# Kernel optimization log

Hardware: AMD Instinct MI355X
Metric: run time of the kernel (lower is better)

## Reference

```python
import jax, jax.numpy as jnp
import numpy as np

N = 30000   # total nodes
E = 240000  # edges
B = 64      # graphs / proteins
H = 10      # GATv2 heads
C = 78      # per-head out dim (= xd_features)
D = H * C   # 780
SEQ = 1000
EMB = 128
LH = 64     # LSTM hidden per direction


def _lstm_dir(xs, Wih, Whh, bih, bhh, reverse):
    # xs: [T, Bn, EMB]; PyTorch gate order i,f,g,o
    Bn = xs.shape[1]
    h0 = jnp.zeros((Bn, LH), xs.dtype)
    def step(carry, xt):
        h, c = carry
        z = xt @ Wih.T + h @ Whh.T + bih + bhh
        i, f, g, o = jnp.split(z, 4, axis=-1)
        c = jax.nn.sigmoid(f) * c + jax.nn.sigmoid(i) * jnp.tanh(g)
        h = jax.nn.sigmoid(o) * jnp.tanh(c)
        return (h, c), h
    _, hs = jax.lax.scan(step, (h0, h0), xs, reverse=reverse)
    return hs


def setup_inputs() -> dict:
    k = jax.random.key(0)
    nxt = lambda i: jax.random.fold_in(k, i)
    s = 0.05
    d = {}
    d['x'] = jax.random.normal(nxt(0), (N, C), jnp.float32)
    d['edge_index'] = jax.random.randint(nxt(1), (2, E), 0, N)
    d['batch'] = jnp.sort(jax.random.randint(nxt(2), (N,), 0, B))
    d['target'] = jax.random.randint(nxt(3), (B, SEQ), 0, 26)
    # GATv2Conv params (share_weights=False)
    d['Wl'] = jax.random.normal(nxt(4), (C, D), jnp.float32) * s
    d['Wr'] = jax.random.normal(nxt(5), (C, D), jnp.float32) * s
    d['att'] = jax.random.normal(nxt(6), (H, C), jnp.float32) * s
    d['gat_b'] = jnp.zeros((D,), jnp.float32)
    # GCNConv params
    d['gcn_w'] = jax.random.normal(nxt(7), (D, D), jnp.float32) * s
    d['gcn_b'] = jnp.zeros((D,), jnp.float32)
    # protein branch
    d['emb'] = jax.random.normal(nxt(8), (26, EMB), jnp.float32) * s
    for tag, base in (('f', 9), ('b', 13)):
        d['Wih_' + tag] = jax.random.normal(nxt(base), (4 * LH, EMB), jnp.float32) * s
        d['Whh_' + tag] = jax.random.normal(nxt(base + 1), (4 * LH, LH), jnp.float32) * s
        d['bih_' + tag] = jnp.zeros((4 * LH,), jnp.float32)
        d['bhh_' + tag] = jnp.zeros((4 * LH,), jnp.float32)
    d['conv_w'] = jax.random.normal(nxt(17), (32, SEQ, 8), jnp.float32) * s
    d['conv_b'] = jnp.zeros((32,), jnp.float32)
    d['fcp_w'] = jax.random.normal(nxt(18), (32 * 121, 128), jnp.float32) * s
    d['fcp_b'] = jnp.zeros((128,), jnp.float32)
    # combined MLP (actual concat dim = 2*780 + 128 = 1688)
    d['fc1_w'] = jax.random.normal(nxt(19), (1688, 1024), jnp.float32) * s
    d['fc1_b'] = jnp.zeros((1024,), jnp.float32)
    d['fc2_w'] = jax.random.normal(nxt(20), (1024, 512), jnp.float32) * s
    d['fc2_b'] = jnp.zeros((512,), jnp.float32)
    d['out_w'] = jax.random.normal(nxt(21), (512, 1), jnp.float32) * s
    d['out_b'] = jnp.zeros((1,), jnp.float32)
    return d


def reference(x, edge_index, batch, target, Wl, Wr, att, gat_b, gcn_w, gcn_b,
              emb, Wih_f, Whh_f, bih_f, bhh_f, Wih_b, Whh_b, bih_b, bhh_b,
              conv_w, conv_b, fcp_w, fcp_b, fc1_w, fc1_b, fc2_w, fc2_b,
              out_w, out_b):
    # ---- graph branch (eval mode: dropout off) ----
    loops = jnp.arange(N)
    src = jnp.concatenate([edge_index[0], loops])  # self loops (PyG default)
    dst = jnp.concatenate([edge_index[1], loops])

    # GATv2Conv
    xl = (x @ Wl).reshape(N, H, C)
    xr = (x @ Wr).reshape(N, H, C)
    e = jax.nn.leaky_relu(xl[src] + xr[dst], 0.2)       # [E+N, H, C]
    logit = jnp.einsum('ehc,hc->eh', e, att)            # [E+N, H]
    m = jax.ops.segment_max(logit, dst, num_segments=N)
    ex = jnp.exp(logit - m[dst])
    den = jax.ops.segment_sum(ex, dst, num_segments=N)
    alpha = ex / den[dst]
    h = jax.ops.segment_sum(alpha[:, :, None] * xl[src], dst, num_segments=N)
    h = jax.nn.elu(h.reshape(N, D) + gat_b)

    # GCNConv with symmetric normalization
    hw = h @ gcn_w
    deg = jax.ops.segment_sum(jnp.ones_like(src, jnp.float32), dst, num_segments=N)
    dinv = jnp.where(deg > 0, jax.lax.rsqrt(jnp.maximum(deg, 1e-12)), 0.0)
    norm = dinv[src] * dinv[dst]
    g = jax.ops.segment_sum(norm[:, None] * hw[src], dst, num_segments=N) + gcn_b
    g = jax.nn.relu(g)

    # global max + mean pooling per graph
    gmax = jax.ops.segment_max(g, batch, num_segments=B)
    cnt = jax.ops.segment_sum(jnp.ones((N,), jnp.float32), batch, num_segments=B)
    gmean = jax.ops.segment_sum(g, batch, num_segments=B) / jnp.maximum(cnt, 1.0)[:, None]
    graph_feat = jnp.concatenate([gmax, gmean], axis=1)  # [B, 1560]

    # ---- protein branch ----
    et = emb[target]                                     # [B, SEQ, EMB]
    # nn.LSTM default batch_first=False: time axis is axis 0 (=B), batch axis is SEQ
    hf = _lstm_dir(et, Wih_f, Whh_f, bih_f, bhh_f, reverse=False)
    hb = _lstm_dir(et, Wih_b, Whh_b, bih_b, bhh_b, reverse=True)
    hcat = jnp.concatenate([hf, hb], axis=-1)            # [B, SEQ, 128]
    conv = jax.lax.conv_general_dilated(hcat, conv_w, (1,), 'VALID',
                                        dimension_numbers=('NCH', 'OIH', 'NCH'))
    conv = conv + conv_b[None, :, None]                  # [B, 32, 121]
    prot = conv.reshape(B, 32 * 121) @ fcp_w + fcp_b     # [B, 128]

    # ---- combined head ----
    comb = jnp.concatenate([graph_feat, prot], axis=1)   # [B, 1688]
    h1 = jax.nn.relu(comb @ fc1_w + fc1_b)
    h2 = jax.nn.relu(h1 @ fc2_w + fc2_b)
    return h2 @ out_w + out_b                            # [B, 1]
```

## Files before the change

### kernel.cpp

```cpp
#include <hip/hip_runtime.h>
#include <hip/hip_bf16.h>
#include <math.h>

static constexpr int NN   = 30000;
static constexpr int EE   = 240000;
static constexpr int ET   = EE + NN;
static constexpr int BB   = 64;
static constexpr int HH   = 10;
static constexpr int CC   = 78;
static constexpr int DD   = HH * CC;
static constexpr int SEQ  = 1000;
static constexpr int EMB  = 128;
static constexpr int LH   = 64;
static constexpr int COMBD = 2 * DD + 128;
static constexpr int PCHUNK = 64;

typedef __attribute__((ext_vector_type(8))) short short8;
typedef __attribute__((ext_vector_type(4))) float f32x4;

__device__ __forceinline__ float bf2f(unsigned short u) {
    return __uint_as_float(((unsigned int)u) << 16);
}

template <int OBF>
__global__ __launch_bounds__(256) void gemm_bf16_mfma(const __hip_bfloat16* __restrict__ A,
                                                      const __hip_bfloat16* __restrict__ Bt,
                                                      void* __restrict__ Cv,
                                                      int M, int N, int K) {
    constexpr int LDS_S = 40;
    __shared__ unsigned short As[128 * LDS_S];
    __shared__ unsigned short Bs[128 * LDS_S];
    const int tid  = threadIdx.x;
    const int lane = tid & 63, wid = tid >> 6;
    const int wr = wid >> 1, wc = wid & 1;
    const int l15 = lane & 15, l4 = lane >> 4;
    const int bm = blockIdx.y * 128, bn = blockIdx.x * 128;
    const int tr = tid >> 2, tc = (tid & 3) * 8;

    const unsigned short* Au = (const unsigned short*)A;
    const unsigned short* Bu = (const unsigned short*)Bt;

    f32x4 acc[4][4];
#pragma unroll
    for (int m = 0; m < 4; ++m)
#pragma unroll
        for (int n = 0; n < 4; ++n) acc[m][n] = (f32x4){0.f, 0.f, 0.f, 0.f};

    for (int k0 = 0; k0 < K; k0 += 32) {
#pragma unroll
        for (int half = 0; half < 2; ++half) {
            int row = tr + half * 64;
            {
                int grow = bm + row;
                short8 sv;
                if (grow < M && k0 + tc + 8 <= K) {
                    const unsigned int* p = (const unsigned int*)(Au + (size_t)grow * K + k0 + tc);
#pragma unroll
                    for (int j = 0; j < 4; ++j) {
                        unsigned int u = p[j];
                        sv[2 * j]     = (short)(u & 0xffffu);
                        sv[2 * j + 1] = (short)(u >> 16);
                    }
                } else {
#pragma unroll
                    for (int j = 0; j < 8; ++j) {
                        int gk = k0 + tc + j;
                        sv[j] = (grow < M && gk < K) ? (short)Au[(size_t)grow * K + gk] : (short)0;
                    }
                }
                *reinterpret_cast<short8*>(&As[row * LDS_S + tc]) = sv;
            }
            {
                int grow = bn + row;
                short8 sv;
                if (grow < N && k0 + tc + 8 <= K) {
                    const unsigned int* p = (const unsigned int*)(Bu + (size_t)grow * K + k0 + tc);
#pragma unroll
                    for (int j = 0; j < 4; ++j) {
                        unsigned int u = p[j];
                        sv[2 * j]     = (short)(u & 0xffffu);
                        sv[2 * j + 1] = (short)(u >> 16);
                    }
                } else {
#pragma unroll
                    for (int j = 0; j < 8; ++j) {
                        int gk = k0 + tc + j;
                        sv[j] = (grow < N && gk < K) ? (short)Bu[(size_t)grow * K + gk] : (short)0;
                    }
                }
                *reinterpret_cast<short8*>(&Bs[row * LDS_S + tc]) = sv;
            }
        }
        __syncthreads();
        short8 a[4], b[4];
#pragma unroll
        for (int m = 0; m < 4; ++m)
            a[m] = *reinterpret_cast<const short8*>(&As[(wr * 64 + m * 16 + l15) * LDS_S + l4 * 8]);
#pragma unroll
        for (int n = 0; n < 4; ++n)
            b[n] = *reinterpret_cast<const short8*>(&Bs[(wc * 64 + n * 16 + l15) * LDS_S + l4 * 8]);
#pragma unroll
        for (int m = 0; m < 4; ++m)
#pragma unroll
            for (int n = 0; n < 4; ++n)
                acc[m][n] = __builtin_amdgcn_mfma_f32_16x16x32_bf16(a[m], b[n], acc[m][n], 0, 0, 0);
        __syncthreads();
    }
#pragma unroll
    for (int m = 0; m < 4; ++m)
#pragma unroll
        for (int n = 0; n < 4; ++n)
#pragma unroll
            for (int r = 0; r < 4; ++r) {
                int row = bm + wr * 64 + m * 16 + l4 * 4 + r;
                int col = bn + wc * 64 + n * 16 + l15;
                if (row < M && col < N) {
                    if (OBF)
                        ((__hip_bfloat16*)Cv)[(size_t)row * N + col] = __float2bfloat16(acc[m][n][r]);
                    else
                        ((float*)Cv)[(size_t)row * N + col] = acc[m][n][r];
                }
            }
}

__global__ void f32_to_bf16(const float* __restrict__ in, __hip_bfloat16* __restrict__ out, int n) {
    int i = blockIdx.x * blockDim.x + threadIdx.x;
    if (i < n) out[i] = __float2bfloat16(in[i]);
}

__global__ void transpose_to_bf16(const float* __restrict__ in, __hip_bfloat16* __restrict__ out,
                                  int Kdim, int Ndim) {
    int idx = blockIdx.x * blockDim.x + threadIdx.x;
    if (idx >= Kdim * Ndim) return;
    int n = idx / Kdim, k = idx % Kdim;
    out[idx] = __float2bfloat16(in[(size_t)k * Ndim + n]);
}

__global__ void transpose_f32(const float* __restrict__ in, float* __restrict__ out,
                              int Kdim, int Ndim) {
    int idx = blockIdx.x * blockDim.x + threadIdx.x;
    if (idx >= Kdim * Ndim) return;
    int n = idx / Kdim, k = idx % Kdim;
    out[idx] = in[(size_t)k * Ndim + n];
}

template <int ACT>
__global__ __launch_bounds__(256) void gemm_skinny(const float* __restrict__ A,
                                                   const float* __restrict__ Bt,
                                                   const float* __restrict__ bias,
                                                   float* __restrict__ C,
                                                   int M, int N, int K, int ldc) {
    int oidx = blockIdx.x * 4 + (threadIdx.x >> 6);
    int lane = threadIdx.x & 63;
    if (oidx >= M * N) return;
    int row = oidx / N, col = oidx % N;
    const float4* a = (const float4*)(A + (size_t)row * K);
    const float4* b = (const float4*)(Bt + (size_t)col * K);
    int K4 = K >> 2;
    float s = 0.f;
    for (int i = lane; i < K4; i += 64) {
        float4 x = a[i], y = b[i];
        s += x.x * y.x + x.y * y.y + x.z * y.z + x.w * y.w;
    }
#pragma unroll
    for (int off = 32; off; off >>= 1) s += __shfl_xor(s, off);
    if (lane == 0) {
        s += bias[col];
        if (ACT == 1) s = fmaxf(s, 0.f);
        C[(size_t)row * ldc + col] = s;
    }
}

__global__ void deg_count(const int* __restrict__ ei, int* __restrict__ deg) {
    int e = blockIdx.x * blockDim.x + threadIdx.x;
    if (e >= ET) return;
    int d = (e < EE) ? ei[EE + e] : (e - EE);
    atomicAdd(&deg[d], 1);
}

__global__ __launch_bounds__(1024) void scan_kernel(const int* __restrict__ deg,
                                                    int* __restrict__ offs) {
    __shared__ int lds[1024];
    int tid = threadIdx.x;
    const int chunk = (NN + 1023) / 1024;
    int base = tid * chunk;
    int s = 0;
    for (int i = 0; i < chunk; ++i) {
        int idx = base + i;
        if (idx < NN) s += deg[idx];
    }
    lds[tid] = s;
    __syncthreads();
    for (int d = 1; d < 1024; d <<= 1) {
        int v = (tid >= d) ? lds[tid - d] : 0;
        __syncthreads();
        lds[tid] += v;
        __syncthreads();
    }
    int run = (tid == 0) ? 0 : lds[tid - 1];
    for (int i = 0; i < chunk; ++i) {
        int idx = base + i;
        if (idx < NN) { offs[idx] = run; run += deg[idx]; }
    }
    if (tid == 1023) offs[NN] = lds[1023];
}

__global__ void csr_fill(const int* __restrict__ ei, const int* __restrict__ offs,
                         int* __restrict__ cursor, int* __restrict__ csr_src,
                         int* __restrict__ csr_dst) {
    int e = blockIdx.x * blockDim.x + threadIdx.x;
    if (e >= ET) return;
    int s = (e < EE) ? ei[e] : (e - EE);
    int d = (e < EE) ? ei[EE + e] : (e - EE);
    int pos = atomicAdd(&cursor[d], 1);
    int slot = offs[d] + pos;
    csr_src[slot] = s;
    csr_dst[slot] = d;
}

__global__ void dinv_kernel(const int* __restrict__ deg, float* __restrict__ dinv) {
    int n = blockIdx.x * blockDim.x + threadIdx.x;
    if (n >= NN) return;
    float dg = (float)deg[n];
    dinv[n] = (dg > 0.f) ? 1.f / sqrtf(dg) : 0.f;
}

__global__ void gat_logits(const unsigned short* __restrict__ xl,
                           const unsigned short* __restrict__ xr,
                           const float* __restrict__ att, const int* __restrict__ csr_src,
                           const int* __restrict__ csr_dst, float* __restrict__ logit) {
    int idx = blockIdx.x * blockDim.x + threadIdx.x;
    if (idx >= ET * HH) return;
    int i = idx / HH, h = idx % HH;
    int s = csr_src[i], d = csr_dst[i];
    const unsigned int* pl = (const unsigned int*)(xl + (size_t)s * DD + h * CC);
    const unsigned int* pr = (const unsigned int*)(xr + (size_t)d * DD + h * CC);
    const float* pa = att + h * CC;
    float acc = 0.f;
#pragma unroll
    for (int c = 0; c < CC / 2; ++c) {
        unsigned int a = pl[c], b = pr[c];
        float v0 = __uint_as_float((a & 0xffffu) << 16) + __uint_as_float((b & 0xffffu) << 16);
        float v1 = __uint_as_float(a & 0xffff0000u) + __uint_as_float(b & 0xffff0000u);
        v0 = (v0 > 0.f) ? v0 : 0.2f * v0;
        v1 = (v1 > 0.f) ? v1 : 0.2f * v1;
        acc += pa[2 * c] * v0 + pa[2 * c + 1] * v1;
    }
    logit[idx] = acc;
}

__global__ void gat_softmax(const int* __restrict__ offs, float* __restrict__ logit) {
    int idx = blockIdx.x * blockDim.x + threadIdx.x;
    if (idx >= NN * HH) return;
    int n = idx / HH, h = idx % HH;
    int i0 = offs[n], i1 = offs[n + 1];
    float m = -1e30f;
    for (int i = i0; i < i1; ++i) m = fmaxf(m, logit[i * HH + h]);
    float den = 0.f;
    for (int i = i0; i < i1; ++i) {
        float e = expf(logit[i * HH + h] - m);
        logit[i * HH + h] = e;
        den += e;
    }
    float inv = 1.f / den;
    for (int i = i0; i < i1; ++i) logit[i * HH + h] *= inv;
}

__global__ __launch_bounds__(256) void gat_aggregate(const int* __restrict__ offs,
                                                     const int* __restrict__ csr_src,
                                                     const float* __restrict__ alpha,
                                                     const unsigned short* __restrict__ xl,
                                                     const float* __restrict__ gat_b,
                                                     __hip_bfloat16* __restrict__ hout) {
    int n = blockIdx.x;
    int tid = threadIdx.x;
    int i0 = offs[n], i1 = offs[n + 1];
    int d0 = tid, d1 = tid + 256, d2 = tid + 512, d3 = tid + 768;
    int h0 = d0 / CC, h1 = d1 / CC, h2 = d2 / CC, h3 = (d3 < DD) ? d3 / CC : 0;
    float a0 = 0.f, a1 = 0.f, a2 = 0.f, a3 = 0.f;
    for (int i = i0; i < i1; ++i) {
        const unsigned short* row = xl + (size_t)csr_src[i] * DD;
        const float* al = alpha + (size_t)i * HH;
        a0 += al[h0] * bf2f(row[d0]);
        a1 += al[h1] * bf2f(row[d1]);
        a2 += al[h2] * bf2f(row[d2]);
        if (d3 < DD) a3 += al[h3] * bf2f(row[d3]);
    }
    float v;
    v = a0 + gat_b[d0]; v = (v > 0.f) ? v : expf(v) - 1.f;
    hout[(size_t)n * DD + d0] = __float2bfloat16(v);
    v = a1 + gat_b[d1]; v = (v > 0.f) ? v : expf(v) - 1.f;
    hout[(size_t)n * DD + d1] = __float2bfloat16(v);
    v = a2 + gat_b[d2]; v = (v > 0.f) ? v : expf(v) - 1.f;
    hout[(size_t)n * DD + d2] = __float2bfloat16(v);
    if (d3 < DD) {
        v = a3 + gat_b[d3]; v = (v > 0.f) ? v : expf(v) - 1.f;
        hout[(size_t)n * DD + d3] = __float2bfloat16(v);
    }
}

__global__ __launch_bounds__(256) void gcn_aggregate(const int* __restrict__ offs,
                                                     const int* __restrict__ csr_src,
                                                     const float* __restrict__ dinv,
                                                     const unsigned short* __restrict__ hw,
                                                     const float* __restrict__ gcn_b,
                                                     __hip_bfloat16* __restrict__ g) {
    int n = blockIdx.x;
    int tid = threadIdx.x;
    float din = dinv[n];
    int i0 = offs[n], i1 = offs[n + 1];
    int d0 = tid, d1 = tid + 256, d2 = tid + 512, d3 = tid + 768;
    float a0 = 0.f, a1 = 0.f, a2 = 0.f, a3 = 0.f;
    for (int i = i0; i < i1; ++i) {
        int s = csr_src[i];
        float w = dinv[s] * din;
        const unsigned short* row = hw + (size_t)s * DD;
        a0 += w * bf2f(row[d0]);
        a1 += w * bf2f(row[d1]);
        a2 += w * bf2f(row[d2]);
        if (d3 < DD) a3 += w * bf2f(row[d3]);
    }
    g[(size_t)n * DD + d0] = __float2bfloat16(fmaxf(a0 + gcn_b[d0], 0.f));
    g[(size_t)n * DD + d1] = __float2bfloat16(fmaxf(a1 + gcn_b[d1], 0.f));
    g[(size_t)n * DD + d2] = __float2bfloat16(fmaxf(a2 + gcn_b[d2], 0.f));
    if (d3 < DD) g[(size_t)n * DD + d3] = __float2bfloat16(fmaxf(a3 + gcn_b[d3], 0.f));
}

__global__ void graph_ranges(const int* __restrict__ batch, int* __restrict__ gstart,
                             int* __restrict__ gend) {
    int n = blockIdx.x * blockDim.x + threadIdx.x;
    if (n >= NN) return;
    int b = batch[n];
    if (n == 0 || batch[n - 1] != b) gstart[b] = n;
    if (n == NN - 1 || batch[n + 1] != b) gend[b] = n + 1;
}

__global__ __launch_bounds__(256) void pool_partial(const unsigned short* __restrict__ g,
                                                    const int* __restrict__ batch,
                                                    float* __restrict__ pmax,
                                                    float* __restrict__ psum) {
    int chunk0 = blockIdx.x * PCHUNK;
    int tid = threadIdx.x;
    __shared__ int bsh[PCHUNK];
    for (int i = tid; i < PCHUNK; i += 256) {
        int n = chunk0 + i;
        bsh[i] = (n < NN) ? batch[n] : -1;
    }
    __syncthreads();
    float mx[4] = {0.f, 0.f, 0.f, 0.f};
    float sm[4] = {0.f, 0.f, 0.f, 0.f};
    int curb = bsh[0];
    auto flush = [&](int b) {
#pragma unroll
        for (int j = 0; j < 4; ++j) {
            int d = tid + j * 256;
            if (d < DD && b >= 0) {
                atomicMax((unsigned int*)&pmax[(size_t)b * DD + d], __float_as_uint(mx[j]));
                atomicAdd(&psum[(size_t)b * DD + d], sm[j]);
            }
            mx[j] = 0.f; sm[j] = 0.f;
        }
    };
    for (int i = 0; i < PCHUNK; ++i) {
        int n = chunk0 + i;
        if (n >= NN) break;
        int b = bsh[i];
        if (b != curb) { flush(curb); curb = b; }
        const unsigned short* row = g + (size_t)n * DD;
#pragma unroll
        for (int j = 0; j < 4; ++j) {
            int d = tid + j * 256;
            if (d < DD) {
                float v = bf2f(row[d]);
                mx[j] = fmaxf(mx[j], v);
                sm[j] += v;
            }
        }
    }
    flush(curb);
}

__global__ void pool_finalize(const float* __restrict__ pmax, const float* __restrict__ psum,
                              const int* __restrict__ gstart, const int* __restrict__ gend,
                              float* __restrict__ comb) {
    int idx = blockIdx.x * blockDim.x + threadIdx.x;
    if (idx >= BB * DD) return;
    int b = idx / DD, d = idx % DD;
    float cnt = fmaxf((float)(gend[b] - gstart[b]), 1.f);
    comb[(size_t)b * COMBD + d] = pmax[idx];
    comb[(size_t)b * COMBD + DD + d] = psum[idx] / cnt;
}

__global__ void proj26_kernel(const float* __restrict__ emb,
                              const float* __restrict__ Wih_f, const float* __restrict__ bih_f,
                              const float* __restrict__ bhh_f,
                              const float* __restrict__ Wih_b, const float* __restrict__ bih_b,
                              const float* __restrict__ bhh_b, float* __restrict__ proj) {
    int dir = blockIdx.x, row = blockIdx.y, j = threadIdx.x;
    const float* W = dir ? Wih_b : Wih_f;
    const float* b1 = dir ? bih_b : bih_f;
    const float* b2 = dir ? bhh_b : bhh_f;
    float acc = b1[j] + b2[j];
    const float* e = emb + row * EMB;
    const float* w = W + j * EMB;
    for (int k = 0; k < EMB; ++k) acc += e[k] * w[k];
    proj[(dir * 26 + row) * 256 + j] = acc;
}

__global__ __launch_bounds__(256) void lstm_kernel(const int* __restrict__ target,
                                                   const float* __restrict__ proj26,
                                                   const float* __restrict__ Whh_f,
                                                   const float* __restrict__ Whh_b,
                                                   float* __restrict__ hcat) {
    int n = blockIdx.x;
    int dir = blockIdx.y;
    int tid = threadIdx.x;
    const float* Whh = dir ? Whh_b : Whh_f;
    const float* proj = proj26 + dir * 26 * 256;
    float w[LH];
#pragma unroll
    for (int u4 = 0; u4 < LH / 4; ++u4) {
        float4 v = *reinterpret_cast<const float4*>(Whh + tid * LH + u4 * 4);
        w[u4 * 4 + 0] = v.x; w[u4 * 4 + 1] = v.y;
        w[u4 * 4 + 2] = v.z; w[u4 * 4 + 3] = v.w;
    }
    __shared__ float h_lds[LH];
    __shared__ float c_lds[LH];
    __shared__ float z_lds[256];
    if (tid < LH) { h_lds[tid] = 0.f; c_lds[tid] = 0.f; }
    __syncthreads();
    for (int s = 0; s < BB; ++s) {
        int t = dir ? (BB - 1 - s) : s;
        int tgt = target[t * SEQ + n];
        float a0 = 0.f, a1 = 0.f, a2 = 0.f, a3 = 0.f;
#pragma unroll
        for (int u = 0; u < LH; u += 4) {
            a0 += w[u] * h_lds[u];
            a1 += w[u + 1] * h_lds[u + 1];
            a2 += w[u + 2] * h_lds[u + 2];
            a3 += w[u + 3] * h_lds[u + 3];
        }
        z_lds[tid] = proj[tgt * 256 + tid] + a0 + a1 + a2 + a3;
        __syncthreads();
        if (tid < LH) {
            float ig = 1.f / (1.f + expf(-z_lds[tid]));
            float fg = 1.f / (1.f + expf(-z_lds[LH + tid]));
            float gg = tanhf(z_lds[2 * LH + tid]);
            float og = 1.f / (1.f + expf(-z_lds[3 * LH + tid]));
            float c = fg * c_lds[tid] + ig * gg;
            float h = og * tanhf(c);
            c_lds[tid] = c;
            h_lds[tid] = h;
            hcat[((size_t)t * SEQ + n) * 128 + dir * LH + tid] = h;
        }
        __syncthreads();
    }
}

__global__ __launch_bounds__(256) void transpose_hcat(const float* __restrict__ hcat,
                                                      unsigned short* __restrict__ hcatT) {
    int b = blockIdx.z;
    int i0 = blockIdx.y * 32;
    int h0 = blockIdx.x * 32;
    int th = threadIdx.x & 31;
    int ti = threadIdx.x >> 5;
    __shared__ float t[32][33];
#pragma unroll
    for (int r = 0; r < 4; ++r) {
        int i = i0 + ti + r * 8;
        if (i < SEQ) t[ti + r * 8][th] = hcat[((size_t)b * SEQ + i) * 128 + h0 + th];
    }
    __syncthreads();
#pragma unroll
    for (int r = 0; r < 4; ++r) {
        int h = h0 + ti + r * 8;
        int i = i0 + th;
        if (i < SEQ) {
            unsigned int u = __float_as_uint(t[th][ti + r * 8]);
            unsigned int lsb = (u >> 16) & 1u;
            u += 0x7fffu + lsb;
            hcatT[((size_t)b * 128 + h) * SEQ + i] = (unsigned short)(u >> 16);
        }
    }
}

__global__ void reshape_convw(const float* __restrict__ conv_w, __hip_bfloat16* __restrict__ wT) {
    int idx = blockIdx.x * blockDim.x + threadIdx.x;
    if (idx >= 256 * SEQ) return;
    int np = idx / SEQ, i = idx % SEQ;
    int o = np >> 3, k = np & 7;
    wT[idx] = __float2bfloat16(conv_w[((size_t)o * SEQ + i) * 8 + k]);
}

__global__ void conv_finalize(const float* __restrict__ T, const float* __restrict__ conv_b,
                              float* __restrict__ convout) {
    int idx = blockIdx.x * blockDim.x + threadIdx.x;
    if (idx >= BB * 32 * 121) return;
    int p = idx % 121;
    int o = (idx / 121) % 32;
    int b = idx / (121 * 32);
    float acc = conv_b[o];
#pragma unroll
    for (int k = 0; k < 8; ++k)
        acc += T[(size_t)(b * 128 + p + k) * 256 + o * 8 + k];
    convout[(size_t)b * 3872 + o * 121 + p] = acc;
}

extern "C" void kernel_launch(void* const* d_in, const int* in_sizes, int n_in,
                              void* d_out, int out_size, void* d_ws, size_t ws_size,
                              hipStream_t stream) {
    const float* x      = (const float*)d_in[0];
    const int*   ei     = (const int*)d_in[1];
    const int*   batch  = (const int*)d_in[2];
    const int*   target = (const int*)d_in[3];
    const float* Wl     = (const float*)d_in[4];
    const float* Wr     = (const float*)d_in[5];
    const float* att    = (const float*)d_in[6];
    const float* gat_b  = (const float*)d_in[7];
    const float* gcn_w  = (const float*)d_in[8];
    const float* gcn_b  = (const float*)d_in[9];
    const float* emb    = (const float*)d_in[10];
    const float* Wih_f  = (const float*)d_in[11];
    const float* Whh_f  = (const float*)d_in[12];
    const float* bih_f  = (const float*)d_in[13];
    const float* bhh_f  = (const float*)d_in[14];
    const float* Wih_b  = (const float*)d_in[15];
    const float* Whh_b  = (const float*)d_in[16];
    const float* bih_b  = (const float*)d_in[17];
    const float* bhh_b  = (const float*)d_in[18];
    const float* conv_w = (const float*)d_in[19];
    const float* conv_b = (const float*)d_in[20];
    const float* fcp_w  = (const float*)d_in[21];
    const float* fcp_b  = (const float*)d_in[22];
    const float* fc1_w  = (const float*)d_in[23];
    const float* fc1_b  = (const float*)d_in[24];
    const float* fc2_w  = (const float*)d_in[25];
    const float* fc2_b  = (const float*)d_in[26];
    const float* out_w  = (const float*)d_in[27];
    const float* out_b  = (const float*)d_in[28];
    float* out = (float*)d_out;
    (void)n_in; (void)in_sizes; (void)out_size;

    char* ws = (char*)d_ws;
    size_t o = 0;
    auto alloc = [&](size_t bytes) {
        char* p = ws + o;
        o = (o + bytes + 255) & ~(size_t)255;
        return p;
    };
    constexpr size_t HALF = (size_t)NN * DD * 2;
    char* region = (char*)alloc(2 * HALF);
    __hip_bfloat16* xl_bf = (__hip_bfloat16*)region;
    __hip_bfloat16* xr_bf = (__hip_bfloat16*)(region + HALF);
    __hip_bfloat16* hw_bf = (__hip_bfloat16*)region;
    __hip_bfloat16* g_bf  = (__hip_bfloat16*)(region + HALF);
    char* rp = region;
    auto palloc = [&](size_t bytes) {
        char* p = rp;
        rp += (bytes + 255) & ~(size_t)255;
        return p;
    };
    float* hcat    = (float*)palloc((size_t)BB * SEQ * 128 * 4);
    float* proj26  = (float*)palloc(2 * 26 * 256 * 4);
    float* convout = (float*)palloc((size_t)BB * 3872 * 4);
    __hip_bfloat16* wT = (__hip_bfloat16*)palloc((size_t)256 * SEQ * 2);
    unsigned short* hcatT = (unsigned short*)palloc((size_t)BB * 128 * SEQ * 2);
    float* T = (float*)palloc((size_t)BB * 128 * 256 * 4);
    __hip_bfloat16* h_bf  = (__hip_bfloat16*)alloc(HALF);
    __hip_bfloat16* x_bf  = (__hip_bfloat16*)alloc((size_t)NN * CC * 2);
    __hip_bfloat16* wl_t  = (__hip_bfloat16*)alloc((size_t)DD * CC * 2);
    __hip_bfloat16* wr_t  = (__hip_bfloat16*)alloc((size_t)DD * CC * 2);
    __hip_bfloat16* gcw_t = (__hip_bfloat16*)alloc((size_t)DD * DD * 2);
    float* fcp_wt = (float*)alloc((size_t)3872 * 128 * 4);
    float* fc1_wt = (float*)alloc((size_t)COMBD * 1024 * 4);
    float* fc2_wt = (float*)alloc((size_t)1024 * 512 * 4);
    float* out_wt = (float*)alloc((size_t)512 * 4);
    float* logit    = (float*)alloc((size_t)ET * HH * 4);
    int*   csr_src  = (int*)alloc((size_t)ET * 4);
    int*   csr_dst  = (int*)alloc((size_t)ET * 4);
    int*   deg      = (int*)alloc((size_t)NN * 4);
    int*   cursor   = (int*)alloc((size_t)NN * 4);
    int*   offs     = (int*)alloc((size_t)(NN + 1) * 4);
    float* dinv     = (float*)alloc((size_t)NN * 4);
    int*   gstart   = (int*)alloc(64 * 4);
    int*   gend     = (int*)alloc(64 * 4);
    float* pmax     = (float*)alloc((size_t)BB * DD * 4);
    float* psum     = (float*)alloc((size_t)BB * DD * 4);
    float* comb     = (float*)alloc((size_t)BB * COMBD * 4);
    float* h1       = (float*)alloc((size_t)BB * 1024 * 4);
    float* h2       = (float*)alloc((size_t)BB * 512 * 4);
    if (o > ws_size) return;

    hipMemsetAsync(deg, 0, (size_t)NN * 4, stream);
    hipMemsetAsync(cursor, 0, (size_t)NN * 4, stream);
    hipMemsetAsync(gstart, 0, 64 * 4, stream);
    hipMemsetAsync(gend, 0, 64 * 4, stream);
    hipMemsetAsync(pmax, 0, (size_t)BB * DD * 4, stream);
    hipMemsetAsync(psum, 0, (size_t)BB * DD * 4, stream);

    {
        dim3 grid(2, 26);
        proj26_kernel<<<grid, 256, 0, stream>>>(emb, Wih_f, bih_f, bhh_f, Wih_b, bih_b, bhh_b, proj26);
    }
    {
        dim3 grid(SEQ, 2);
        lstm_kernel<<<grid, 256, 0, stream>>>(target, proj26, Whh_f, Whh_b, hcat);
    }
    {
        dim3 grid(4, 32, BB);
        transpose_hcat<<<grid, 256, 0, stream>>>(hcat, hcatT);
    }
    reshape_convw<<<(256 * SEQ + 255) / 256, 256, 0, stream>>>(conv_w, wT);
    {
        dim3 grid(2, 64);
        gemm_bf16_mfma<0><<<grid, 256, 0, stream>>>((const __hip_bfloat16*)hcatT, wT, T,
                                                    BB * 128, 256, SEQ);
    }
    conv_finalize<<<(BB * 32 * 121 + 255) / 256, 256, 0, stream>>>(T, conv_b, convout);
    transpose_f32<<<(3872 * 128 + 255) / 256, 256, 0, stream>>>(fcp_w, fcp_wt, 3872, 128);
    gemm_skinny<0><<<(BB * 128 + 3) / 4, 256, 0, stream>>>(convout, fcp_wt, fcp_b,
                                                           comb + 2 * DD, BB, 128, 3872, COMBD);

    f32_to_bf16<<<(NN * CC + 255) / 256, 256, 0, stream>>>(x, x_bf, NN * CC);
    transpose_to_bf16<<<(CC * DD + 255) / 256, 256, 0, stream>>>(Wl, wl_t, CC, DD);
    transpose_to_bf16<<<(CC * DD + 255) / 256, 256, 0, stream>>>(Wr, wr_t, CC, DD);
    transpose_to_bf16<<<(DD * DD + 255) / 256, 256, 0, stream>>>(gcn_w, gcw_t, DD, DD);
    transpose_f32<<<(COMBD * 1024 + 255) / 256, 256, 0, stream>>>(fc1_w, fc1_wt, COMBD, 1024);
    transpose_f32<<<(1024 * 512 + 255) / 256, 256, 0, stream>>>(fc2_w, fc2_wt, 1024, 512);
    transpose_f32<<<(512 + 255) / 256, 256, 0, stream>>>(out_w, out_wt, 512, 1);

    dim3 ggrid((DD + 127) / 128, (NN + 127) / 128);
    gemm_bf16_mfma<1><<<ggrid, 256, 0, stream>>>(x_bf, wl_t, xl_bf, NN, DD, CC);
    gemm_bf16_mfma<1><<<ggrid, 256, 0, stream>>>(x_bf, wr_t, xr_bf, NN, DD, CC);
    deg_count<<<(ET + 255) / 256, 256, 0, stream>>>(ei, deg);
    scan_kernel<<<1, 1024, 0, stream>>>(deg, offs);
    csr_fill<<<(ET + 255) / 256, 256, 0, stream>>>(ei, offs, cursor, csr_src, csr_dst);
    dinv_kernel<<<(NN + 255) / 256, 256, 0, stream>>>(deg, dinv);
    gat_logits<<<(ET * HH + 255) / 256, 256, 0, stream>>>((const unsigned short*)xl_bf,
                                                          (const unsigned short*)xr_bf,
                                                          att, csr_src, csr_dst, logit);
    gat_softmax<<<(NN * HH + 255) / 256, 256, 0, stream>>>(offs, logit);
    gat_aggregate<<<NN, 256, 0, stream>>>(offs, csr_src, logit,
                                          (const unsigned short*)xl_bf, gat_b, h_bf);
    gemm_bf16_mfma<1><<<ggrid, 256, 0, stream>>>(h_bf, gcw_t, hw_bf, NN, DD, DD);
    gcn_aggregate<<<NN, 256, 0, stream>>>(offs, csr_src, dinv,
                                          (const unsigned short*)hw_bf, gcn_b, g_bf);
    graph_ranges<<<(NN + 255) / 256, 256, 0, stream>>>(batch, gstart, gend);
    pool_partial<<<(NN + PCHUNK - 1) / PCHUNK, 256, 0, stream>>>((const unsigned short*)g_bf,
                                                                 batch, pmax, psum);
    pool_finalize<<<(BB * DD + 255) / 256, 256, 0, stream>>>(pmax, psum, gstart, gend, comb);

    gemm_skinny<1><<<(BB * 1024 + 3) / 4, 256, 0, stream>>>(comb, fc1_wt, fc1_b, h1,
                                                            BB, 1024, COMBD, 1024);
    gemm_skinny<1><<<(BB * 512 + 3) / 4, 256, 0, stream>>>(h1, fc2_wt, fc2_b, h2,
                                                           BB, 512, 1024, 512);
    gemm_skinny<0><<<(BB + 3) / 4, 256, 0, stream>>>(h2, out_wt, out_b, out,
                                                     BB, 1, 512, 1);
}
```

Baseline: 1.009 ms.

## Fuse GAT logits, softmax and aggregation into one per-node kernel with online softmax

Replaces the three GAT kernels (per-edge logits, per-node softmax, aggregation) with one per-node kernel. It stages each chunk of up to 32 neighbour xl rows in LDS, computes the logits there and applies an online softmax with rescaling. The goal is to drop the logit buffer round trips and read each neighbour row from global memory once instead of twice. It also remaps GEMM workgroup IDs so contiguous tiles land on the same XCD, for better L2 reuse. The risks are a large LDS footprint (about 55 KB), which limits occupancy, and the logit phase using only tsz*10 active threads.

```diff
diff --git a/kernel.cpp b/kernel.cpp
--- a/kernel.cpp
+++ b/kernel.cpp
@@ -14,6 +14,7 @@
 static constexpr int LH   = 64;
 static constexpr int COMBD = 2 * DD + 128;
 static constexpr int PCHUNK = 64;
+static constexpr int DEGC = 32;
 
 typedef __attribute__((ext_vector_type(8))) short short8;
 typedef __attribute__((ext_vector_type(4))) float f32x4;
@@ -34,7 +35,15 @@
     const int lane = tid & 63, wid = tid >> 6;
     const int wr = wid >> 1, wc = wid & 1;
     const int l15 = lane & 15, l4 = lane >> 4;
-    const int bm = blockIdx.y * 128, bn = blockIdx.x * 128;
+    int l = blockIdx.y * gridDim.x + blockIdx.x;
+    {
+        int nwg = gridDim.x * gridDim.y;
+        int q = nwg >> 3, r = nwg & 7;
+        int xcd = l & 7, idx = l >> 3;
+        l = (xcd < r) ? (xcd * (q + 1) + idx) : (r * (q + 1) + (xcd - r) * q + idx);
+    }
+    const int bm = (l / gridDim.x) * 128;
+    const int bn = (l % gridDim.x) * 128;
     const int tr = tid >> 2, tc = (tid & 3) * 8;
 
     const unsigned short* Au = (const unsigned short*)A;
@@ -225,77 +234,97 @@
     dinv[n] = (dg > 0.f) ? 1.f / sqrtf(dg) : 0.f;
 }
 
-__global__ void gat_logits(const unsigned short* __restrict__ xl,
-                           const unsigned short* __restrict__ xr,
-                           const float* __restrict__ att, const int* __restrict__ csr_src,
-                           const int* __restrict__ csr_dst, float* __restrict__ logit) {
-    int idx = blockIdx.x * blockDim.x + threadIdx.x;
-    if (idx >= ET * HH) return;
-    int i = idx / HH, h = idx % HH;
-    int s = csr_src[i], d = csr_dst[i];
-    const unsigned int* pl = (const unsigned int*)(xl + (size_t)s * DD + h * CC);
-    const unsigned int* pr = (const unsigned int*)(xr + (size_t)d * DD + h * CC);
-    const float* pa = att + h * CC;
-    float acc = 0.f;
-#pragma unroll
-    for (int c = 0; c < CC / 2; ++c) {
-        unsigned int a = pl[c], b = pr[c];
-        float v0 = __uint_as_float((a & 0xffffu) << 16) + __uint_as_float((b & 0xffffu) << 16);
-        float v1 = __uint_as_float(a & 0xffff0000u) + __uint_as_float(b & 0xffff0000u);
-        v0 = (v0 > 0.f) ? v0 : 0.2f * v0;
-        v1 = (v1 > 0.f) ? v1 : 0.2f * v1;
-        acc += pa[2 * c] * v0 + pa[2 * c + 1] * v1;
-    }
-    logit[idx] = acc;
-}
-
-__global__ void gat_softmax(const int* __restrict__ offs, float* __restrict__ logit) {
-    int idx = blockIdx.x * blockDim.x + threadIdx.x;
-    if (idx >= NN * HH) return;
-    int n = idx / HH, h = idx % HH;
-    int i0 = offs[n], i1 = offs[n + 1];
-    float m = -1e30f;
-    for (int i = i0; i < i1; ++i) m = fmaxf(m, logit[i * HH + h]);
-    float den = 0.f;
-    for (int i = i0; i < i1; ++i) {
-        float e = expf(logit[i * HH + h] - m);
-        logit[i * HH + h] = e;
-        den += e;
-    }
-    float inv = 1.f / den;
-    for (int i = i0; i < i1; ++i) logit[i * HH + h] *= inv;
-}
-
-__global__ __launch_bounds__(256) void gat_aggregate(const int* __restrict__ offs,
-                                                     const int* __restrict__ csr_src,
-                                                     const float* __restrict__ alpha,
-                                                     const unsigned short* __restrict__ xl,
-                                                     const float* __restrict__ gat_b,
-                                                     __hip_bfloat16* __restrict__ hout) {
-    int n = blockIdx.x;
-    int tid = threadIdx.x;
-    int i0 = offs[n], i1 = offs[n + 1];
-    int d0 = tid, d1 = tid + 256, d2 = tid + 512, d3 = tid + 768;
-    int h0 = d0 / CC, h1 = d1 / CC, h2 = d2 / CC, h3 = (d3 < DD) ? d3 / CC : 0;
-    float a0 = 0.f, a1 = 0.f, a2 = 0.f, a3 = 0.f;
-    for (int i = i0; i < i1; ++i) {
-        const unsigned short* row = xl + (size_t)csr_src[i] * DD;
-        const float* al = alpha + (size_t)i * HH;
-        a0 += al[h0] * bf2f(row[d0]);
-        a1 += al[h1] * bf2f(row[d1]);
-        a2 += al[h2] * bf2f(row[d2]);
-        if (d3 < DD) a3 += al[h3] * bf2f(row[d3]);
-    }
-    float v;
-    v = a0 + gat_b[d0]; v = (v > 0.f) ? v : expf(v) - 1.f;
-    hout[(size_t)n * DD + d0] = __float2bfloat16(v);
-    v = a1 + gat_b[d1]; v = (v > 0.f) ? v : expf(v) - 1.f;
-    hout[(size_t)n * DD + d1] = __float2bfloat16(v);
-    v = a2 + gat_b[d2]; v = (v > 0.f) ? v : expf(v) - 1.f;
-    hout[(size_t)n * DD + d2] = __float2bfloat16(v);
-    if (d3 < DD) {
-        v = a3 + gat_b[d3]; v = (v > 0.f) ? v : expf(v) - 1.f;
-        hout[(size_t)n * DD + d3] = __float2bfloat16(v);
+__global__ __launch_bounds__(256) void gat_fused(const int* __restrict__ offs,
+                                                 const int* __restrict__ csr_src,
+                                                 const unsigned short* __restrict__ xl,
+                                                 const unsigned short* __restrict__ xr,
+                                                 const float* __restrict__ att,
+                                                 const float* __restrict__ gat_b,
+                                                 __hip_bfloat16* __restrict__ hout) {
+    __shared__ float att_s[DD];
+    __shared__ unsigned short xr_s[DD];
+    __shared__ unsigned short xl_s[DEGC * DD];
+    __shared__ float lg[DEGC * HH];
+    __shared__ int srcs[DEGC];
+    __shared__ float m_s[HH], l_s[HH], fac_s[HH];
+    const int n = blockIdx.x;
+    const int tid = threadIdx.x;
+    const int i0 = offs[n], deg = offs[n + 1] - i0;
+
+    for (int j = tid; j < DD; j += 256) att_s[j] = att[j];
+    {
+        const unsigned int* sp = (const unsigned int*)(xr + (size_t)n * DD);
+        unsigned int* dp = (unsigned int*)xr_s;
+        for (int j = tid; j < DD / 2; j += 256) dp[j] = sp[j];
+    }
+    if (tid < HH) { m_s[tid] = -1e30f; l_s[tid] = 0.f; }
+
+    int d_[4], h_[4];
+#pragma unroll
+    for (int j = 0; j < 4; ++j) {
+        d_[j] = tid + j * 256;
+        h_[j] = (d_[j] < DD) ? d_[j] / CC : 0;
+    }
+    float acc[4] = {0.f, 0.f, 0.f, 0.f};
+
+    for (int t0 = 0; t0 < deg; t0 += DEGC) {
+        int tsz = min(DEGC, deg - t0);
+        __syncthreads();
+        if (tid < tsz) srcs[tid] = csr_src[i0 + t0 + tid];
+        __syncthreads();
+        int total = tsz * (DD / 2);
+        for (int j = tid; j < total; j += 256) {
+            int e = j / (DD / 2), c = j - e * (DD / 2);
+            ((unsigned int*)xl_s)[e * (DD / 2) + c] =
+                ((const unsigned int*)(xl + (size_t)srcs[e] * DD))[c];
+        }
+        __syncthreads();
+        for (int t = tid; t < tsz * HH; t += 256) {
+            int e = t / HH, h = t - e * HH;
+            const unsigned short* xe  = &xl_s[e * DD + h * CC];
+            const unsigned short* xrp = &xr_s[h * CC];
+            const float* at = &att_s[h * CC];
+            float s = 0.f;
+            for (int c = 0; c < CC; ++c) {
+                float v = bf2f(xe[c]) + bf2f(xrp[c]);
+                v = (v > 0.f) ? v : 0.2f * v;
+                s += at[c] * v;
+            }
+            lg[e * HH + h] = s;
+        }
+        __syncthreads();
+        if (tid < HH) {
+            float mx = m_s[tid];
+            for (int e = 0; e < tsz; ++e) mx = fmaxf(mx, lg[e * HH + tid]);
+            float f = __expf(m_s[tid] - mx);
+            float sum = l_s[tid] * f;
+            for (int e = 0; e < tsz; ++e) {
+                float p = __expf(lg[e * HH + tid] - mx);
+                lg[e * HH + tid] = p;
+                sum += p;
+            }
+            m_s[tid] = mx; l_s[tid] = sum; fac_s[tid] = f;
+        }
+        __syncthreads();
+#pragma unroll
+        for (int j = 0; j < 4; ++j) {
+            int d = d_[j];
+            if (d < DD) {
+                float a = acc[j] * fac_s[h_[j]];
+                for (int e = 0; e < tsz; ++e)
+                    a += lg[e * HH + h_[j]] * bf2f(xl_s[e * DD + d]);
+                acc[j] = a;
+            }
+        }
+    }
+#pragma unroll
+    for (int j = 0; j < 4; ++j) {
+        int d = d_[j];
+        if (d < DD) {
+            float v = acc[j] / l_s[h_[j]] + gat_b[d];
+            v = (v > 0.f) ? v : __expf(v) - 1.f;
+            hout[(size_t)n * DD + d] = __float2bfloat16(v);
+        }
     }
 }
 
@@ -575,7 +604,6 @@
     float* fc1_wt = (float*)alloc((size_t)COMBD * 1024 * 4);
     float* fc2_wt = (float*)alloc((size_t)1024 * 512 * 4);
     float* out_wt = (float*)alloc((size_t)512 * 4);
-    float* logit    = (float*)alloc((size_t)ET * HH * 4);
     int*   csr_src  = (int*)alloc((size_t)ET * 4);
     int*   csr_dst  = (int*)alloc((size_t)ET * 4);
     int*   deg      = (int*)alloc((size_t)NN * 4);
@@ -636,12 +664,10 @@
     scan_kernel<<<1, 1024, 0, stream>>>(deg, offs);
     csr_fill<<<(ET + 255) / 256, 256, 0, stream>>>(ei, offs, cursor, csr_src, csr_dst);
     dinv_kernel<<<(NN + 255) / 256, 256, 0, stream>>>(deg, dinv);
-    gat_logits<<<(ET * HH + 255) / 256, 256, 0, stream>>>((const unsigned short*)xl_bf,
-                                                          (const unsigned short*)xr_bf,
-                                                          att, csr_src, csr_dst, logit);
-    gat_softmax<<<(NN * HH + 255) / 256, 256, 0, stream>>>(offs, logit);
-    gat_aggregate<<<NN, 256, 0, stream>>>(offs, csr_src, logit,
-                                          (const unsigned short*)xl_bf, gat_b, h_bf);
+    gat_fused<<<NN, 256, 0, stream>>>(offs, csr_src,
+                                      (const unsigned short*)xl_bf,
+                                      (const unsigned short*)xr_bf,
+                                      att, gat_b, h_bf);
     gemm_bf16_mfma<1><<<ggrid, 256, 0, stream>>>(h_bf, gcw_t, hw_bf, NN, DD, DD);
     gcn_aggregate<<<NN, 256, 0, stream>>>(offs, csr_src, dinv,
                                           (const unsigned short*)hw_bf, gcn_b, g_bf);
```

Result: slower. 1.241 ms (+23.0%).
